# Performance work log

Measured on AMD Instinct MI355X. Metric: run time of the kernel, lower is better.

The kernel has to match this reference:

```python
import jax, jax.numpy as jnp
import numpy as np

NUM_HEADS = 12

def setup_inputs() -> dict:
    key = jax.random.key(0)
    ks = jax.random.split(key, 6)
    B, Nq, Nkv, C = 2, 2048, 2048, 768
    q_token = jax.random.normal(ks[0], (B, Nq, C), dtype=jnp.float32)
    kv_token = jax.random.normal(ks[1], (B, Nkv, C), dtype=jnp.float32)
    s = 1.0 / np.sqrt(C)
    Wq = jax.random.normal(ks[2], (C, C), dtype=jnp.float32) * s
    Wkv = jax.random.normal(ks[3], (C, 2 * C), dtype=jnp.float32) * s
    Wproj = jax.random.normal(ks[4], (C, C), dtype=jnp.float32) * s
    bproj = jnp.zeros((C,), dtype=jnp.float32)
    return {"q_token": q_token, "kv_token": kv_token, "Wq": Wq, "Wkv": Wkv, "Wproj": Wproj, "bproj": bproj}

def reference(q_token, kv_token, Wq, Wkv, Wproj, bproj):
    B, Nq, C = q_token.shape
    H = NUM_HEADS
    D = C // H
    scale = D ** -0.5
    # Q: [B, H, Nq, D]
    Q = (q_token @ Wq).reshape(B, Nq, H, D).transpose(0, 2, 1, 3)
    # KV: token layout is (2, H, D) on last dim -> [2, B, H, Nkv, D]
    Nkv = kv_token.shape[1]
    KV = (kv_token @ Wkv).reshape(B, Nkv, 2, H, D).transpose(2, 0, 3, 1, 4)
    K, V = KV[0], KV[1]
    attn = jnp.einsum('bhqd,bhkd->bhqk', Q, K) * scale
    attn = jax.nn.softmax(attn, axis=-1)
    # NOTE: original code multiplies by scale again here (faithful quirk)
    x = jnp.einsum('bhqk,bhkd->bhqd', attn, V) * scale
    x = x.transpose(0, 2, 1, 3).reshape(B, Nq, C)
    return x @ Wproj + bproj
```

## Files before the change

kernel.cpp:

```cpp
#include <hip/hip_runtime.h>

typedef __attribute__((ext_vector_type(8))) short short8;
typedef __attribute__((ext_vector_type(4))) float f32x4;
typedef __attribute__((ext_vector_type(16))) float f32x16;
typedef __attribute__((ext_vector_type(4))) unsigned u32x4;

__device__ __forceinline__ unsigned short f2bf(float f) {
  unsigned u = __builtin_bit_cast(unsigned, f);
  u += 0x7fffu + ((u >> 16) & 1u);
  return (unsigned short)(u >> 16);
}

__device__ __forceinline__ unsigned cvt_pk_bf16(float a, float b) {
  unsigned r;
  asm("v_cvt_pk_bf16_f32 %0, %1, %2" : "=v"(r) : "v"(a), "v"(b));
  return r;
}

__device__ __forceinline__ void gload_lds16(const unsigned short* g, unsigned short* l) {
  __builtin_amdgcn_global_load_lds((const __attribute__((address_space(1))) unsigned int*)g,
                                   (__attribute__((address_space(3))) unsigned int*)l, 16, 0, 0);
}

__global__ __launch_bounds__(256) void cvt_tr(
    const float* __restrict__ q_token, const float* __restrict__ kv_token,
    const float* __restrict__ Wq, const float* __restrict__ Wkv, const float* __restrict__ Wp,
    unsigned short* __restrict__ qb, unsigned short* __restrict__ kvb,
    unsigned short* __restrict__ wqT, unsigned short* __restrict__ wkvT,
    unsigned short* __restrict__ wpT) {
  __shared__ float tile[32][33];
  const int tid = threadIdx.x;
  int bx = blockIdx.x;
  if (bx < 6144) {
    int i = bx * 256 + tid;
    const float* in = (i < 786432) ? q_token : kv_token;
    unsigned short* out = (i < 786432) ? qb : kvb;
    int j = (i < 786432) ? i : i - 786432;
    float4 v = ((const float4*)in)[j];
    ushort4 o;
    o.x = f2bf(v.x); o.y = f2bf(v.y); o.z = f2bf(v.z); o.w = f2bf(v.w);
    ((ushort4*)out)[j] = o;
    return;
  }
  bx -= 6144;
  int gx = bx % 96, gy = bx / 96;
  const float* in; unsigned short* out; int C;
  if (gx < 24)       { in = Wq;  out = wqT;  C = 768;  }
  else if (gx < 72)  { in = Wkv; out = wkvT; C = 1536; gx -= 24; }
  else               { in = Wp;  out = wpT;  C = 768;  gx -= 72; }
  const int R = 768;
  int c0 = gx * 32, r0 = gy * 32;
  int tx = tid & 31, ty = tid >> 5;
  for (int i = ty; i < 32; i += 8)
    tile[i][tx] = in[(size_t)(r0 + i) * C + c0 + tx];
  __syncthreads();
  for (int i = ty; i < 32; i += 8)
    out[(size_t)(c0 + i) * R + r0 + tx] = f2bf(tile[tx][i]);
}

__global__ __launch_bounds__(256) void gemm_qkv(
    const unsigned short* __restrict__ Aq, const unsigned short* __restrict__ Akv,
    const unsigned short* __restrict__ BtQ, const unsigned short* __restrict__ BtKV,
    unsigned short* __restrict__ Qo, unsigned short* __restrict__ Ko,
    unsigned short* __restrict__ Vo) {
  __shared__ __align__(16) unsigned short A_lds[128][64];
  __shared__ __align__(16) unsigned short B_lds[64][64];
  const bool isQ = blockIdx.y < 12;
  const unsigned short* A  = isQ ? Aq : Akv;
  const unsigned short* Bt = isQ ? BtQ : BtKV;
  const int yy = isQ ? blockIdx.y : blockIdx.y - 12;
  const int K = 768;
  const int tile_m = blockIdx.x * 128;
  const int tile_n = yy * 64;
  const int tid = threadIdx.x;
  const int wid = tid >> 6, lane = tid & 63;
  const int wm = (wid >> 1) * 64, wn = (wid & 1) * 32;
  const int lr = lane & 15, lg = lane >> 4;
  const int s_row = (lane >> 3);
  const int s_col = (lane & 7) * 8;
  f32x4 acc[4][2] = {};

  for (int k0 = 0; k0 < K; k0 += 64) {
    __syncthreads();
#pragma unroll
    for (int j = 0; j < 6; ++j) {
      const int c = wid * 6 + j;
      if (c < 16) {
        const int row = c * 8 + s_row;
        gload_lds16(&A[(size_t)(tile_m + row) * K + k0 + s_col], &A_lds[0][0] + c * 512);
      } else {
        const int row = (c - 16) * 8 + s_row;
        gload_lds16(&Bt[(size_t)(tile_n + row) * K + k0 + s_col], &B_lds[0][0] + (c - 16) * 512);
      }
    }
    __syncthreads();
    short8 a[4][2], b[2][2];
#pragma unroll
    for (int i = 0; i < 4; ++i)
#pragma unroll
      for (int t = 0; t < 2; ++t)
        a[i][t] = *(const short8*)&A_lds[wm + i * 16 + lr][t * 32 + lg * 8];
#pragma unroll
    for (int j = 0; j < 2; ++j)
#pragma unroll
      for (int t = 0; t < 2; ++t)
        b[j][t] = *(const short8*)&B_lds[wn + j * 16 + lr][t * 32 + lg * 8];
#pragma unroll
    for (int i = 0; i < 4; ++i)
#pragma unroll
      for (int j = 0; j < 2; ++j)
#pragma unroll
        for (int t = 0; t < 2; ++t)
          acc[i][j] = __builtin_amdgcn_mfma_f32_16x16x32_bf16(a[i][t], b[j][t], acc[i][j], 0, 0, 0);
  }

#pragma unroll
  for (int i = 0; i < 4; ++i)
#pragma unroll
    for (int j = 0; j < 2; ++j)
#pragma unroll
      for (int r = 0; r < 4; ++r) {
        int m = tile_m + wm + i * 16 + lg * 4 + r;
        int n = tile_n + wn + j * 16 + lr;
        float v = acc[i][j][r];
        int b = m >> 11, row = m & 2047;
        if (isQ) {
          int h = n >> 6, d = n & 63;
          Qo[((size_t)((b * 12 + h) * 2048 + row) << 6) + d] = f2bf(v);
        } else {
          if (n < 768) {
            int h = n >> 6, d = n & 63;
            Ko[((size_t)((b * 12 + h) * 2048 + row) << 6) + d] = f2bf(v);
          } else {
            int h = (n - 768) >> 6, d = n & 63;
            int rowp = (row & ~12) | ((row & 4) << 1) | ((row & 8) >> 1);
            int tile = rowp >> 6, poff = rowp & 63;
            int ss = poff >> 4, hh = (poff >> 3) & 1, ee = poff & 7;
            Vo[(size_t)(b * 12 + h) * 131072 + tile * 4096 +
               ((ss * 2 + hh) * 64 + d) * 8 + ee] = f2bf(v);
          }
        }
      }
}

__global__ __launch_bounds__(256) void gemm_proj(
    const unsigned short* __restrict__ A, const unsigned short* __restrict__ Bt,
    float* __restrict__ outf, const float* __restrict__ bias) {
  __shared__ __align__(16) unsigned short A_lds[64][64];
  __shared__ __align__(16) unsigned short B_lds[64][64];
  const int K = 768, N = 768;
  const int tile_m = blockIdx.x * 64;
  const int tile_n = blockIdx.y * 64;
  const int tid = threadIdx.x;
  const int wid = tid >> 6, lane = tid & 63;
  const int wm = (wid >> 1) * 32, wn = (wid & 1) * 32;
  const int lr = lane & 15, lg = lane >> 4;
  const int s_r8 = lane >> 3;
  const int s_col = (lane & 7) * 8;
  f32x4 acc[2][2] = {};

  for (int k0 = 0; k0 < K; k0 += 64) {
    __syncthreads();
#pragma unroll
    for (int i = 0; i < 2; ++i) {
      const int row = (wid * 2 + i) * 8 + s_r8;
      gload_lds16(&A[(size_t)(tile_m + row) * K + k0 + s_col], &A_lds[0][0] + (wid * 2 + i) * 512);
      gload_lds16(&Bt[(size_t)(tile_n + row) * K + k0 + s_col], &B_lds[0][0] + (wid * 2 + i) * 512);
    }
    __syncthreads();
    short8 a[2][2], b[2][2];
#pragma unroll
    for (int i = 0; i < 2; ++i)
#pragma unroll
      for (int t = 0; t < 2; ++t) {
        a[i][t] = *(const short8*)&A_lds[wm + i * 16 + lr][t * 32 + lg * 8];
        b[i][t] = *(const short8*)&B_lds[wn + i * 16 + lr][t * 32 + lg * 8];
      }
#pragma unroll
    for (int i = 0; i < 2; ++i)
#pragma unroll
      for (int j = 0; j < 2; ++j)
#pragma unroll
        for (int t = 0; t < 2; ++t)
          acc[i][j] = __builtin_amdgcn_mfma_f32_16x16x32_bf16(a[i][t], b[j][t], acc[i][j], 0, 0, 0);
  }

#pragma unroll
  for (int i = 0; i < 2; ++i)
#pragma unroll
    for (int j = 0; j < 2; ++j)
#pragma unroll
      for (int r = 0; r < 4; ++r) {
        int m = tile_m + wm + i * 16 + lg * 4 + r;
        int n = tile_n + wn + j * 16 + lr;
        outf[(size_t)m * N + n] = acc[i][j][r] + bias[n];
      }
}

__global__ __launch_bounds__(256, 3) void attn_fwd(
    const unsigned short* __restrict__ Q, const unsigned short* __restrict__ Kb,
    const unsigned short* __restrict__ Vt, unsigned short* __restrict__ X) {
  __shared__ __align__(16) unsigned short SMEM[16384];
  __shared__ float m_lds[4][32];
  __shared__ float l_lds[4][64];
  const int bid = blockIdx.x;
  const int bh = bid % 24;
  const int q0 = (bid / 24) * 64;
  const int tid = threadIdx.x, wid = tid >> 6, lane = tid & 63;
  const int l31 = lane & 31, hi = lane >> 5;
  const int grp = wid >> 1;
  const int qsub = wid & 1;
  const float Cc = 0.18033688011112042f;
  const float THRS = 44.3614195558365f;

  const unsigned short* Kbase = Kb + (size_t)bh * (2048 * 64);
  const unsigned short* Vbase = Vt + (size_t)bh * 131072;

  short8 qf[4];
  {
    const unsigned short* Qp = Q + ((size_t)bh * 2048 + q0 + qsub * 32 + l31) * 64 + hi * 8;
#pragma unroll
    for (int t = 0; t < 4; ++t) qf[t] = *(const short8*)&Qp[t * 16];
  }

  f32x16 accO0 = {}, accO1 = {};
  float m_run = -1e30f, l_run = 0.f;

  const int gtid = tid & 127;
  const int s_row = gtid >> 3;
  const int s_chk = gtid & 7;
  unsigned short* Kst0 = SMEM + grp * 8192;
  unsigned short* Kst1 = SMEM + grp * 8192 + 4096;
  const int fr = l31 & 7;

  {
    const int kvb = grp * 1024;
#pragma unroll
    for (int p = 0; p < 4; ++p) {
      const int row = p * 16 + s_row;
      float4 v = *(const float4*)&Kbase[(size_t)(kvb + row) * 64 + s_chk * 8];
      *(float4*)&Kst0[row * 64 + ((s_chk ^ (row & 7)) << 3)] = v;
    }
  }
  __syncthreads();

  for (int t = 0; t < 16; ++t) {
    const int cur = t & 1;
    const int kv0 = grp * 1024 + t * 64;
    float4 nK[4];
    if (t < 15) {
#pragma unroll
      for (int p = 0; p < 4; ++p) {
        const int row = p * 16 + s_row;
        nK[p] = *(const float4*)&Kbase[(size_t)(kv0 + 64 + row) * 64 + s_chk * 8];
      }
    }
    short8 vf[8];
    {
      const unsigned short* Vtile = Vbase + (kv0 >> 6) * 4096;
#pragma unroll
      for (int s = 0; s < 4; ++s) {
        const unsigned short* seg = Vtile + (s * 2 + hi) * 512;
        vf[s]     = *(const short8*)&seg[l31 * 8];
        vf[4 + s] = *(const short8*)&seg[(32 + l31) * 8];
      }
    }
    const unsigned short* KL = cur ? Kst1 : Kst0;
    f32x16 S0 = {}, S1 = {};
    __builtin_amdgcn_s_setprio(1);
#pragma unroll
    for (int t4 = 0; t4 < 4; ++t4) {
      const int ca = ((2 * t4 + hi) ^ fr) << 3;
      short8 k0 = *(const short8*)&KL[l31 * 64 + ca];
      short8 k1 = *(const short8*)&KL[(32 + l31) * 64 + ca];
      S0 = __builtin_amdgcn_mfma_f32_32x32x16_bf16(k0, qf[t4], S0, 0, 0, 0);
      S1 = __builtin_amdgcn_mfma_f32_32x32x16_bf16(k1, qf[t4], S1, 0, 0, 0);
    }
    __builtin_amdgcn_s_setprio(0);
    float mx[8];
#pragma unroll
    for (int g = 0; g < 4; ++g) {
      mx[g]     = fmaxf(fmaxf(S0[4 * g], S0[4 * g + 1]), fmaxf(S0[4 * g + 2], S0[4 * g + 3]));
      mx[4 + g] = fmaxf(fmaxf(S1[4 * g], S1[4 * g + 1]), fmaxf(S1[4 * g + 2], S1[4 * g + 3]));
    }
    float rmax = fmaxf(fmaxf(fmaxf(mx[0], mx[1]), fmaxf(mx[2], mx[3])),
                       fmaxf(fmaxf(mx[4], mx[5]), fmaxf(mx[6], mx[7])));
    rmax = fmaxf(rmax, __shfl_xor(rmax, 32));
    if (!__all(rmax <= m_run + THRS)) {
      float mnew = fmaxf(m_run, rmax);
      float alpha = exp2f((m_run - mnew) * Cc);
      m_run = mnew;
      l_run *= alpha;
#pragma unroll
      for (int r = 0; r < 16; ++r) { accO0[r] *= alpha; accO1[r] *= alpha; }
    }
    const float mC = m_run * Cc;
#pragma unroll
    for (int r = 0; r < 16; ++r) {
      S0[r] = exp2f(fmaf(S0[r], Cc, -mC));
      S1[r] = exp2f(fmaf(S1[r], Cc, -mC));
    }
    float ts[8];
#pragma unroll
    for (int g = 0; g < 4; ++g) {
      ts[g]     = (S0[4 * g] + S0[4 * g + 1]) + (S0[4 * g + 2] + S0[4 * g + 3]);
      ts[4 + g] = (S1[4 * g] + S1[4 * g + 1]) + (S1[4 * g + 2] + S1[4 * g + 3]);
    }
    l_run += ((ts[0] + ts[1]) + (ts[2] + ts[3])) + ((ts[4] + ts[5]) + (ts[6] + ts[7]));
    unsigned w0[8], w1[8];
#pragma unroll
    for (int j = 0; j < 4; ++j) {
      w0[j]     = cvt_pk_bf16(S0[4 * j],     S0[4 * j + 1]);
      w1[j]     = cvt_pk_bf16(S0[4 * j + 2], S0[4 * j + 3]);
      w0[4 + j] = cvt_pk_bf16(S1[4 * j],     S1[4 * j + 1]);
      w1[4 + j] = cvt_pk_bf16(S1[4 * j + 2], S1[4 * j + 3]);
    }
    __builtin_amdgcn_s_setprio(1);
#pragma unroll
    for (int s = 0; s < 4; ++s) {
      u32x4 pw = {w0[2 * s], w1[2 * s], w0[2 * s + 1], w1[2 * s + 1]};
      short8 pfrag = __builtin_bit_cast(short8, pw);
      accO0 = __builtin_amdgcn_mfma_f32_32x32x16_bf16(vf[s], pfrag, accO0, 0, 0, 0);
      accO1 = __builtin_amdgcn_mfma_f32_32x32x16_bf16(vf[4 + s], pfrag, accO1, 0, 0, 0);
    }
    __builtin_amdgcn_s_setprio(0);
    if (t < 15) {
      unsigned short* KN = cur ? Kst0 : Kst1;
#pragma unroll
      for (int p = 0; p < 4; ++p) {
        const int row = p * 16 + s_row;
        *(float4*)&KN[row * 64 + ((s_chk ^ (row & 7)) << 3)] = nK[p];
      }
    }
    __syncthreads();
  }

  float* Ob = (float*)SMEM;
#pragma unroll
  for (int dt = 0; dt < 2; ++dt) {
    const f32x16& acc = dt ? accO1 : accO0;
#pragma unroll
    for (int r = 0; r < 16; ++r)
      Ob[wid * 2048 + (dt * 16 + r) * 64 + hi * 32 + l31] = acc[r];
  }
  if (hi == 0) m_lds[wid][l31] = m_run;
  l_lds[wid][hi * 32 + l31] = l_run;
  __syncthreads();

  {
    const int qs = wid >> 1, dh = wid & 1;
    const int sl0 = qs, sl1 = qs + 2;
    float m0 = m_lds[sl0][l31], m1 = m_lds[sl1][l31];
    float M = fmaxf(m0, m1);
    float w0s = exp2f((m0 - M) * Cc);
    float w1s = exp2f((m1 - M) * Cc);
    float ltot = w0s * (l_lds[sl0][l31] + l_lds[sl0][32 + l31])
               + w1s * (l_lds[sl1][l31] + l_lds[sl1][32 + l31]);
    const float inv = 0.125f / ltot;
    const int b = bh / 12, h = bh % 12;
    short8 os0, os1;
#pragma unroll
    for (int j = 0; j < 16; ++j) {
      const int d = dh * 32 + hi * 16 + j;
      const int dt = d >> 5, crow = d & 31;
      const int hs = (crow >> 2) & 1;
      const int rr = (crow & 3) | ((crow >> 3) << 2);
      float v = w0s * Ob[sl0 * 2048 + (dt * 16 + rr) * 64 + hs * 32 + l31]
              + w1s * Ob[sl1 * 2048 + (dt * 16 + rr) * 64 + hs * 32 + l31];
      if (j < 8) os0[j] = (short)f2bf(v * inv);
      else       os1[j - 8] = (short)f2bf(v * inv);
    }
    const int q = q0 + qs * 32 + l31;
    unsigned short* Xp = X + ((size_t)b * 2048 + q) * 768 + h * 64 + dh * 32 + hi * 16;
    *(short8*)Xp = os0;
    *(short8*)(Xp + 8) = os1;
  }
}

extern "C" void kernel_launch(void* const* d_in, const int* in_sizes, int n_in,
                              void* d_out, int out_size, void* d_ws, size_t ws_size,
                              hipStream_t stream) {
  const float* q_token  = (const float*)d_in[0];
  const float* kv_token = (const float*)d_in[1];
  const float* Wq    = (const float*)d_in[2];
  const float* Wkv   = (const float*)d_in[3];
  const float* Wproj = (const float*)d_in[4];
  const float* bproj = (const float*)d_in[5];
  float* out = (float*)d_out;

  unsigned short* qb   = (unsigned short*)d_ws;
  unsigned short* kvb  = qb   + 3145728;
  unsigned short* wqT  = kvb  + 3145728;
  unsigned short* wkvT = wqT  + 589824;
  unsigned short* wpT  = wkvT + 1179648;
  unsigned short* Qb   = wpT  + 589824;
  unsigned short* Kbf  = Qb   + 3145728;
  unsigned short* Vtb  = Kbf  + 3145728;
  unsigned short* Xb   = Vtb  + 3145728;

  cvt_tr<<<8448, 256, 0, stream>>>(q_token, kv_token, Wq, Wkv, Wproj,
                                   qb, kvb, wqT, wkvT, wpT);

  gemm_qkv<<<dim3(32, 36), 256, 0, stream>>>(qb, kvb, wqT, wkvT, Qb, Kbf, Vtb);

  attn_fwd<<<768, 256, 0, stream>>>(Qb, Kbf, Vtb, Xb);

  gemm_proj<<<dim3(64, 12), 256, 0, stream>>>(Xb, wpT, out, bproj);
}
```

Baseline: 108.9 us.

## Store K in MFMA-fragment tiled layout and load directly into registers

```diff
diff --git a/kernel.cpp b/kernel.cpp
--- a/kernel.cpp
+++ b/kernel.cpp
@@ -128,13 +128,17 @@
           int h = n >> 6, d = n & 63;
           Qo[((size_t)((b * 12 + h) * 2048 + row) << 6) + d] = f2bf(v);
         } else {
+          int tile = row >> 6;
           if (n < 768) {
             int h = n >> 6, d = n & 63;
-            Ko[((size_t)((b * 12 + h) * 2048 + row) << 6) + d] = f2bf(v);
+            int kvo = row & 63;
+            int t4 = d >> 4, hh = (d >> 3) & 1, ee = d & 7;
+            Ko[(size_t)(b * 12 + h) * 131072 + tile * 4096 +
+               ((t4 * 2 + hh) * 64 + kvo) * 8 + ee] = f2bf(v);
           } else {
             int h = (n - 768) >> 6, d = n & 63;
             int rowp = (row & ~12) | ((row & 4) << 1) | ((row & 8) >> 1);
-            int tile = rowp >> 6, poff = rowp & 63;
+            int poff = rowp & 63;
             int ss = poff >> 4, hh = (poff >> 3) & 1, ee = poff & 7;
             Vo[(size_t)(b * 12 + h) * 131072 + tile * 4096 +
                ((ss * 2 + hh) * 64 + d) * 8 + ee] = f2bf(v);
@@ -200,7 +204,7 @@
 __global__ __launch_bounds__(256, 3) void attn_fwd(
     const unsigned short* __restrict__ Q, const unsigned short* __restrict__ Kb,
     const unsigned short* __restrict__ Vt, unsigned short* __restrict__ X) {
-  __shared__ __align__(16) unsigned short SMEM[16384];
+  __shared__ __align__(16) float Ob[4][32][64];
   __shared__ float m_lds[4][32];
   __shared__ float l_lds[4][64];
   const int bid = blockIdx.x;
@@ -213,7 +217,7 @@
   const float Cc = 0.18033688011112042f;
   const float THRS = 44.3614195558365f;
 
-  const unsigned short* Kbase = Kb + (size_t)bh * (2048 * 64);
+  const unsigned short* Kbase = Kb + (size_t)bh * 131072;
   const unsigned short* Vbase = Vt + (size_t)bh * 131072;
 
   short8 qf[4];
@@ -226,55 +230,26 @@
   f32x16 accO0 = {}, accO1 = {};
   float m_run = -1e30f, l_run = 0.f;
 
-  const int gtid = tid & 127;
-  const int s_row = gtid >> 3;
-  const int s_chk = gtid & 7;
-  unsigned short* Kst0 = SMEM + grp * 8192;
-  unsigned short* Kst1 = SMEM + grp * 8192 + 4096;
-  const int fr = l31 & 7;
-
-  {
-    const int kvb = grp * 1024;
-#pragma unroll
-    for (int p = 0; p < 4; ++p) {
-      const int row = p * 16 + s_row;
-      float4 v = *(const float4*)&Kbase[(size_t)(kvb + row) * 64 + s_chk * 8];
-      *(float4*)&Kst0[row * 64 + ((s_chk ^ (row & 7)) << 3)] = v;
-    }
-  }
-  __syncthreads();
-
   for (int t = 0; t < 16; ++t) {
-    const int cur = t & 1;
-    const int kv0 = grp * 1024 + t * 64;
-    float4 nK[4];
-    if (t < 15) {
-#pragma unroll
-      for (int p = 0; p < 4; ++p) {
-        const int row = p * 16 + s_row;
-        nK[p] = *(const float4*)&Kbase[(size_t)(kv0 + 64 + row) * 64 + s_chk * 8];
-      }
-    }
-    short8 vf[8];
-    {
-      const unsigned short* Vtile = Vbase + (kv0 >> 6) * 4096;
-#pragma unroll
-      for (int s = 0; s < 4; ++s) {
-        const unsigned short* seg = Vtile + (s * 2 + hi) * 512;
-        vf[s]     = *(const short8*)&seg[l31 * 8];
-        vf[4 + s] = *(const short8*)&seg[(32 + l31) * 8];
-      }
-    }
-    const unsigned short* KL = cur ? Kst1 : Kst0;
+    const int tile = grp * 16 + t;
+    const unsigned short* Ktile = Kbase + tile * 4096;
+    const unsigned short* Vtile = Vbase + tile * 4096;
+    short8 kA[8], vf[8];
+#pragma unroll
+    for (int s = 0; s < 4; ++s) {
+      const unsigned short* kseg = Ktile + (s * 2 + hi) * 512;
+      kA[s]     = *(const short8*)&kseg[l31 * 8];
+      kA[4 + s] = *(const short8*)&kseg[(32 + l31) * 8];
+      const unsigned short* vseg = Vtile + (s * 2 + hi) * 512;
+      vf[s]     = *(const short8*)&vseg[l31 * 8];
+      vf[4 + s] = *(const short8*)&vseg[(32 + l31) * 8];
+    }
     f32x16 S0 = {}, S1 = {};
     __builtin_amdgcn_s_setprio(1);
 #pragma unroll
     for (int t4 = 0; t4 < 4; ++t4) {
-      const int ca = ((2 * t4 + hi) ^ fr) << 3;
-      short8 k0 = *(const short8*)&KL[l31 * 64 + ca];
-      short8 k1 = *(const short8*)&KL[(32 + l31) * 64 + ca];
-      S0 = __builtin_amdgcn_mfma_f32_32x32x16_bf16(k0, qf[t4], S0, 0, 0, 0);
-      S1 = __builtin_amdgcn_mfma_f32_32x32x16_bf16(k1, qf[t4], S1, 0, 0, 0);
+      S0 = __builtin_amdgcn_mfma_f32_32x32x16_bf16(kA[t4], qf[t4], S0, 0, 0, 0);
+      S1 = __builtin_amdgcn_mfma_f32_32x32x16_bf16(kA[4 + t4], qf[t4], S1, 0, 0, 0);
     }
     __builtin_amdgcn_s_setprio(0);
     float mx[8];
@@ -324,24 +299,14 @@
       accO1 = __builtin_amdgcn_mfma_f32_32x32x16_bf16(vf[4 + s], pfrag, accO1, 0, 0, 0);
     }
     __builtin_amdgcn_s_setprio(0);
-    if (t < 15) {
-      unsigned short* KN = cur ? Kst0 : Kst1;
-#pragma unroll
-      for (int p = 0; p < 4; ++p) {
-        const int row = p * 16 + s_row;
-        *(float4*)&KN[row * 64 + ((s_chk ^ (row & 7)) << 3)] = nK[p];
-      }
-    }
-    __syncthreads();
-  }
-
-  float* Ob = (float*)SMEM;
+  }
+
 #pragma unroll
   for (int dt = 0; dt < 2; ++dt) {
     const f32x16& acc = dt ? accO1 : accO0;
 #pragma unroll
     for (int r = 0; r < 16; ++r)
-      Ob[wid * 2048 + (dt * 16 + r) * 64 + hi * 32 + l31] = acc[r];
+      Ob[wid][dt * 16 + r][hi * 32 + l31] = acc[r];
   }
   if (hi == 0) m_lds[wid][l31] = m_run;
   l_lds[wid][hi * 32 + l31] = l_run;
@@ -365,8 +330,8 @@
       const int dt = d >> 5, crow = d & 31;
       const int hs = (crow >> 2) & 1;
       const int rr = (crow & 3) | ((crow >> 3) << 2);
-      float v = w0s * Ob[sl0 * 2048 + (dt * 16 + rr) * 64 + hs * 32 + l31]
-              + w1s * Ob[sl1 * 2048 + (dt * 16 + rr) * 64 + hs * 32 + l31];
+      float v = w0s * Ob[sl0][dt * 16 + rr][hs * 32 + l31]
+              + w1s * Ob[sl1][dt * 16 + rr][hs * 32 + l31];
       if (j < 8) os0[j] = (short)f2bf(v * inv);
       else       os1[j - 8] = (short)f2bf(v * inv);
     }
```

New measurement: 106.1 us (median of 2 runs). 1.03x faster.
